# Optimization experiments

Measured on AMD Instinct MI355X. Metric: run time of the kernel, lower is better.

The kernel has to match this reference:

```python
import jax, jax.numpy as jnp
import numpy as np

B, S, H, NH, HD = 8, 1024, 1024, 16, 64
VALID = 512  # valid tokens per sequence (ragged: each seq half-full)
T = B * VALID  # total_nnz
ROPE_THETA = 10000.0
NEG_INF = -1e9


def rotate_half(x):
    x1, x2 = jnp.split(x, 2, axis=-1)
    return jnp.concatenate((-x2, x1), axis=-1)


def setup_inputs() -> dict:
    key = jax.random.key(0)
    k_h, k_qw, k_ow = jax.random.split(key, 3)
    hidden_states = jax.random.normal(k_h, (T, H), jnp.float32)
    # RoPE cos/sin tables at the positions of the unpadded tokens
    inv_freq = 1.0 / (ROPE_THETA ** (np.arange(0, HD, 2, dtype=np.float32) / HD))  # (HD/2,)
    pos = np.tile(np.arange(VALID, dtype=np.float32), B)  # (T,)
    freqs = pos[:, None] * inv_freq[None, :]  # (T, HD/2)
    emb = np.concatenate([freqs, freqs], axis=-1)  # (T, HD)
    cos = jnp.asarray(np.cos(emb))[:, None, :]  # (T, 1, HD) broadcast over heads
    sin = jnp.asarray(np.sin(emb))[:, None, :]
    # indices of valid tokens in the flattened (B*S) padded layout
    indices = jnp.asarray((np.arange(B)[:, None] * S + np.arange(VALID)[None, :]).reshape(-1).astype(np.int64))
    # additive attention bias: 0 for valid keys, -1e9 for padding keys, shape (B,1,1,S)
    key_valid = np.zeros((B, S), dtype=bool)
    key_valid[:, :VALID] = True
    attention_bias = jnp.where(jnp.asarray(key_valid)[:, None, None, :], 0.0, NEG_INF).astype(jnp.float32)
    qkv_w = jax.random.normal(k_qw, (H, 3 * H), jnp.float32) * 0.02
    qkv_b = jnp.zeros((3 * H,), jnp.float32)
    o_w = jax.random.normal(k_ow, (H, H), jnp.float32) * 0.02
    o_b = jnp.zeros((H,), jnp.float32)
    return {"hidden_states": hidden_states, "cos": cos, "sin": sin,
            "attention_bias": attention_bias, "qkv_w": qkv_w, "qkv_b": qkv_b,
            "o_w": o_w, "o_b": o_b, "indices": indices, "batch": B, "seqlen": S}


def reference(hidden_states, cos, sin, attention_bias, qkv_w, qkv_b, o_w, o_b, indices, batch, seqlen):
    # packed QKV projection on unpadded tokens: (T, 3H)
    qkv = hidden_states @ qkv_w + qkv_b
    q, k, v = jnp.split(qkv, 3, axis=-1)
    q = q.reshape(-1, NH, HD)
    k = k.reshape(-1, NH, HD)
    v = v.reshape(-1, NH, HD)
    # rotary position embedding (applied to unpadded q/k)
    q = q * cos + rotate_half(q) * sin
    k = k * cos + rotate_half(k) * sin

    def pad(x):  # (T, NH, HD) -> (B, S, NH, HD), scatter into zero-padded layout
        return jnp.zeros((batch * seqlen, NH, HD), x.dtype).at[indices].set(x).reshape(batch, seqlen, NH, HD)

    qh = pad(q).transpose(0, 2, 1, 3)  # (B, NH, S, HD)
    kh = pad(k).transpose(0, 2, 1, 3)
    vh = pad(v).transpose(0, 2, 1, 3)
    # scaled dot-product attention with additive bias
    scores = jnp.einsum('bhqd,bhkd->bhqk', qh, kh) / jnp.sqrt(jnp.array(HD, qh.dtype)) + attention_bias
    probs = jax.nn.softmax(scores, axis=-1)
    ctx = jnp.einsum('bhqk,bhkd->bhqd', probs, vh)  # (B, NH, S, HD)
    # unpad and merge heads: gather valid rows from flattened (B*S, H)
    out = ctx.transpose(0, 2, 1, 3).reshape(batch * seqlen, NH * HD)[indices]
    return out @ o_w + o_b  # (T, H)
```

## Files before the change

kernel.cpp:

```cpp
#include <hip/hip_runtime.h>

#define T_TOK 4096
#define HDIM  1024
#define NHEAD 16
#define HEADD 64
#define BATCH 8
#define NVALID 512
#define H3    3072

typedef __bf16 bf16;
typedef __attribute__((ext_vector_type(8))) __bf16 bf16x8;
typedef __attribute__((ext_vector_type(4))) __bf16 bf16x4;
typedef __attribute__((ext_vector_type(4))) float f32x4;

__device__ __forceinline__ void load_lds16(const void* g, void* l) {
  __builtin_amdgcn_global_load_lds(
      (const __attribute__((address_space(1))) unsigned int*)g,
      (__attribute__((address_space(3))) unsigned int*)l, 16, 0, 0);
}

__global__ __launch_bounds__(256) void k_cvt(const float* __restrict__ in,
                                             bf16* __restrict__ out) {
  int i = (blockIdx.x * 256 + threadIdx.x) * 4;
  float4 v = *(const float4*)(in + i);
  bf16x4 o;
  o[0] = (bf16)v.x; o[1] = (bf16)v.y; o[2] = (bf16)v.z; o[3] = (bf16)v.w;
  *(bf16x4*)(out + i) = o;
}

__global__ __launch_bounds__(256) void k_tcvt(const float* __restrict__ W,
                                              bf16* __restrict__ Wt,
                                              int K, int N) {
  __shared__ float t[32][33];
  const int ct = blockIdx.x, rt = blockIdx.y;
  const int c = threadIdx.x & 31, r0 = threadIdx.x >> 5;
#pragma unroll
  for (int kk = 0; kk < 4; ++kk) {
    int r = r0 + kk * 8;
    t[r][c] = W[(size_t)(rt * 32 + r) * N + ct * 32 + c];
  }
  __syncthreads();
#pragma unroll
  for (int kk = 0; kk < 4; ++kk) {
    int n = r0 + kk * 8;
    Wt[(size_t)(ct * 32 + n) * K + rt * 32 + c] = (bf16)t[c][n];
  }
}

template <typename OutT>
__global__ __launch_bounds__(256) void k_gemm(const bf16* __restrict__ A,
                                              const bf16* __restrict__ Bt,
                                              const float* __restrict__ bias,
                                              OutT* __restrict__ C,
                                              int M, int N, int K) {
  __shared__ bf16 As[128 * 32];
  __shared__ bf16 Bs[128 * 32];
  const int tid = threadIdx.x;
  const int lane = tid & 63;
  const int wave = tid >> 6;
  const int wr = wave >> 1, wc = wave & 1;
  const int l15 = lane & 15, g = lane >> 4;
  const int row0 = blockIdx.x * 128, col0 = blockIdx.y * 128;

  f32x4 acc[4][4] = {};

  const bf16* Ag = A + (size_t)(row0 + (tid >> 2)) * K + (tid & 3) * 8;
  const bf16* Bg = Bt + (size_t)(col0 + (tid >> 2)) * K + (tid & 3) * 8;
  const int ldsoff = wave * 64 * 8;

  for (int k0 = 0; k0 < K; k0 += 32) {
    __syncthreads();
    load_lds16(Ag + k0, As + ldsoff);
    load_lds16(Ag + k0 + (size_t)64 * K, As + 2048 + ldsoff);
    load_lds16(Bg + k0, Bs + ldsoff);
    load_lds16(Bg + k0 + (size_t)64 * K, Bs + 2048 + ldsoff);
    __syncthreads();

    bf16x8 af[4], bfr[4];
#pragma unroll
    for (int i = 0; i < 4; ++i)
      af[i] = *(const bf16x8*)(As + (wr * 64 + i * 16 + l15) * 32 + g * 8);
#pragma unroll
    for (int j = 0; j < 4; ++j)
      bfr[j] = *(const bf16x8*)(Bs + (wc * 64 + j * 16 + l15) * 32 + g * 8);
#pragma unroll
    for (int i = 0; i < 4; ++i)
#pragma unroll
      for (int j = 0; j < 4; ++j)
        acc[i][j] = __builtin_amdgcn_mfma_f32_16x16x32_bf16(af[i], bfr[j],
                                                            acc[i][j], 0, 0, 0);
  }

#pragma unroll
  for (int i = 0; i < 4; ++i) {
#pragma unroll
    for (int j = 0; j < 4; ++j) {
      int gc = col0 + wc * 64 + j * 16 + l15;
      float bv = bias ? bias[gc] : 0.f;
#pragma unroll
      for (int e = 0; e < 4; ++e) {
        int gr = row0 + wr * 64 + i * 16 + g * 4 + e;
        C[(size_t)gr * N + gc] = (OutT)(acc[i][j][e] + bv);
      }
    }
  }
}

__global__ __launch_bounds__(256) void k_rope(const bf16* __restrict__ qkv,
                                              const float* __restrict__ cosT,
                                              const float* __restrict__ sinT,
                                              bf16* __restrict__ Qr,
                                              bf16* __restrict__ Kr,
                                              bf16* __restrict__ Vt) {
  __shared__ bf16 vt[64][72];
  const int blk = blockIdx.x;
  const int tt = blk & 7, h = (blk >> 3) & 15, b = blk >> 7;
  const int tid = threadIdx.x;
  const int r = tid >> 2, q4 = tid & 3;
  const int d0 = q4 * 8;
  const int t = b * NVALID + tt * 64 + r;
  const size_t qrow = (size_t)t * H3;

  bf16x8 qlo = *(const bf16x8*)(qkv + qrow + h * 64 + d0);
  bf16x8 qhi = *(const bf16x8*)(qkv + qrow + h * 64 + d0 + 32);
  bf16x8 klo = *(const bf16x8*)(qkv + qrow + 1024 + h * 64 + d0);
  bf16x8 khi = *(const bf16x8*)(qkv + qrow + 1024 + h * 64 + d0 + 32);
  bf16x8 vlo = *(const bf16x8*)(qkv + qrow + 2048 + h * 64 + d0);
  bf16x8 vhi = *(const bf16x8*)(qkv + qrow + 2048 + h * 64 + d0 + 32);

  const float* cp = cosT + (size_t)t * 64 + d0;
  const float* sp = sinT + (size_t)t * 64 + d0;
  float clo[8], chi[8], slo[8], shi[8];
  {
    float4 a0 = *(const float4*)cp,        a1 = *(const float4*)(cp + 4);
    float4 b0 = *(const float4*)(cp + 32), b1 = *(const float4*)(cp + 36);
    float4 e0 = *(const float4*)sp,        e1 = *(const float4*)(sp + 4);
    float4 f0 = *(const float4*)(sp + 32), f1 = *(const float4*)(sp + 36);
    clo[0]=a0.x; clo[1]=a0.y; clo[2]=a0.z; clo[3]=a0.w;
    clo[4]=a1.x; clo[5]=a1.y; clo[6]=a1.z; clo[7]=a1.w;
    chi[0]=b0.x; chi[1]=b0.y; chi[2]=b0.z; chi[3]=b0.w;
    chi[4]=b1.x; chi[5]=b1.y; chi[6]=b1.z; chi[7]=b1.w;
    slo[0]=e0.x; slo[1]=e0.y; slo[2]=e0.z; slo[3]=e0.w;
    slo[4]=e1.x; slo[5]=e1.y; slo[6]=e1.z; slo[7]=e1.w;
    shi[0]=f0.x; shi[1]=f0.y; shi[2]=f0.z; shi[3]=f0.w;
    shi[4]=f1.x; shi[5]=f1.y; shi[6]=f1.z; shi[7]=f1.w;
  }

  bf16x8 qo0, qo1, ko0, ko1;
#pragma unroll
  for (int i = 0; i < 8; ++i) {
    float ql = (float)qlo[i], qh = (float)qhi[i];
    float kl = (float)klo[i], kh = (float)khi[i];
    qo0[i] = (bf16)(ql * clo[i] - qh * slo[i]);
    qo1[i] = (bf16)(qh * chi[i] + ql * shi[i]);
    ko0[i] = (bf16)(kl * clo[i] - kh * slo[i]);
    ko1[i] = (bf16)(kh * chi[i] + kl * shi[i]);
  }
  const size_t orow = ((size_t)(b * NHEAD + h) * NVALID + tt * 64 + r) * HEADD;
  *(bf16x8*)(Qr + orow + d0) = qo0;
  *(bf16x8*)(Qr + orow + d0 + 32) = qo1;
  *(bf16x8*)(Kr + orow + d0) = ko0;
  *(bf16x8*)(Kr + orow + d0 + 32) = ko1;

  *(bf16x8*)(&vt[r][d0]) = vlo;
  *(bf16x8*)(&vt[r][d0 + 32]) = vhi;
  __syncthreads();
  const int d = tid >> 2;
  const size_t vbase =
      ((size_t)(b * NHEAD + h) * HEADD + d) * NVALID + tt * 64 + q4 * 16;
  bf16x8 o0, o1;
#pragma unroll
  for (int kk = 0; kk < 8; ++kk) o0[kk] = vt[q4 * 16 + kk][d];
#pragma unroll
  for (int kk = 0; kk < 8; ++kk) o1[kk] = vt[q4 * 16 + 8 + kk][d];
  *(bf16x8*)(Vt + vbase) = o0;
  *(bf16x8*)(Vt + vbase + 8) = o1;
}

__global__ __launch_bounds__(256) void k_attn(const bf16* __restrict__ Qr,
                                              const bf16* __restrict__ Kr,
                                              const bf16* __restrict__ Vt,
                                              bf16* __restrict__ ctx) {
  __shared__ bf16 Ks[128 * 64];
  __shared__ bf16 Vs[64 * 128];
  __shared__ bf16 Ps[4][16 * 136];

  const int blk = blockIdx.x;
  const int qt = blk & 7, h = (blk >> 3) & 15, b = blk >> 7;
  const int tid = threadIdx.x;
  const int lane = tid & 63;
  const int wave = tid >> 6;
  const int l15 = lane & 15, g = lane >> 4;

  const size_t bh = (size_t)(b * NHEAD + h);
  const bf16* Qg = Qr + (bh * NVALID + qt * 64 + wave * 16) * HEADD;
  const bf16* Kg = Kr + bh * NVALID * HEADD;
  const bf16* Vg = Vt + bh * HEADD * NVALID;

  bf16x8 qf0 = *(const bf16x8*)(Qg + l15 * HEADD + g * 8);
  bf16x8 qf1 = *(const bf16x8*)(Qg + l15 * HEADD + 32 + g * 8);

  f32x4 acc[4] = {};
  float mrow[4], srow[4];
#pragma unroll
  for (int e = 0; e < 4; ++e) { mrow[e] = -1e30f; srow[e] = 0.f; }

  const int srK = tid >> 3;
  const int sdK = (tid & 7) << 4;
  const int sdV = tid >> 4;
  const int skV = (tid & 15) << 4;

  bf16* pw = &Ps[wave][0];

  for (int kb = 0; kb < 4; ++kb) {
    __syncthreads();
#pragma unroll
    for (int p = 0; p < 4; ++p) {
      int row = p * 32 + srK;
      int d2 = sdK ^ ((row & 7) << 4);
      load_lds16(Kg + (size_t)(kb * 128 + row) * HEADD + (d2 >> 1),
                 (char*)Ks + (p * 256 + wave * 64) * 16);
    }
#pragma unroll
    for (int p = 0; p < 4; ++p) {
      int d = p * 16 + sdV;
      int k2 = skV ^ ((d & 7) << 4);
      load_lds16(Vg + (size_t)d * NVALID + kb * 128 + (k2 >> 1),
                 (char*)Vs + (p * 256 + wave * 64) * 16);
    }
    __syncthreads();

    f32x4 sc[8];
#pragma unroll
    for (int f = 0; f < 8; ++f) {
      int krow = f * 16 + l15;
      int swz = (krow & 7) << 4;
      const char* kbase = (const char*)Ks + krow * 128;
      bf16x8 kf0 = *(const bf16x8*)(kbase + ((g * 16) ^ swz));
      bf16x8 kf1 = *(const bf16x8*)(kbase + ((g * 16 + 64) ^ swz));
      f32x4 s = {};
      s = __builtin_amdgcn_mfma_f32_16x16x32_bf16(qf0, kf0, s, 0, 0, 0);
      s = __builtin_amdgcn_mfma_f32_16x16x32_bf16(qf1, kf1, s, 0, 0, 0);
      sc[f] = s;
    }

#pragma unroll
    for (int e = 0; e < 4; ++e) {
      float tm = -1e30f;
#pragma unroll
      for (int f = 0; f < 8; ++f) tm = fmaxf(tm, sc[f][e]);
#pragma unroll
      for (int m = 1; m < 16; m <<= 1) tm = fmaxf(tm, __shfl_xor(tm, m, 64));
      tm *= 0.125f;
      float mnew = fmaxf(mrow[e], tm);
      float corr = __expf(mrow[e] - mnew);
      mrow[e] = mnew;
      srow[e] *= corr;
#pragma unroll
      for (int j = 0; j < 4; ++j) acc[j][e] *= corr;
      float rs = 0.f;
#pragma unroll
      for (int f = 0; f < 8; ++f) {
        float p = __expf(sc[f][e] * 0.125f - mnew);
        sc[f][e] = p;
        rs += p;
      }
#pragma unroll
      for (int m = 1; m < 16; m <<= 1) rs += __shfl_xor(rs, m, 64);
      srow[e] += rs;
    }

#pragma unroll
    for (int f = 0; f < 8; ++f)
#pragma unroll
      for (int e = 0; e < 4; ++e)
        pw[(g * 4 + e) * 136 + f * 16 + l15] = (bf16)sc[f][e];

#pragma unroll
    for (int kt = 0; kt < 4; ++kt) {
      bf16x8 pf = *(const bf16x8*)(pw + l15 * 136 + kt * 32 + g * 8);
#pragma unroll
      for (int j = 0; j < 4; ++j) {
        int d = j * 16 + l15;
        int inner = (kt * 64 + g * 16) ^ ((d & 7) << 4);
        bf16x8 vf = *(const bf16x8*)((const char*)Vs + d * 256 + inner);
        acc[j] = __builtin_amdgcn_mfma_f32_16x16x32_bf16(pf, vf, acc[j], 0, 0, 0);
      }
    }
  }

#pragma unroll
  for (int e = 0; e < 4; ++e) {
    float inv = 1.f / srow[e];
    int row = qt * 64 + wave * 16 + g * 4 + e;
    size_t obase = ((size_t)b * NVALID + row) * HDIM + h * HEADD;
#pragma unroll
    for (int j = 0; j < 4; ++j)
      ctx[obase + j * 16 + l15] = (bf16)(acc[j][e] * inv);
  }
}

extern "C" void kernel_launch(void* const* d_in, const int* in_sizes, int n_in,
                              void* d_out, int out_size, void* d_ws, size_t ws_size,
                              hipStream_t stream) {
  const float* hidden = (const float*)d_in[0];
  const float* cosT   = (const float*)d_in[1];
  const float* sinT   = (const float*)d_in[2];
  const float* qkv_w  = (const float*)d_in[4];
  const float* qkv_b  = (const float*)d_in[5];
  const float* o_w    = (const float*)d_in[6];
  const float* o_b    = (const float*)d_in[7];
  float* out = (float*)d_out;

  char* ws = (char*)d_ws;
  const size_t MB = 1024 * 1024;
  bf16* hb  = (bf16*)(ws);
  bf16* w1t = (bf16*)(ws + 8 * MB);
  bf16* w2t = (bf16*)(ws + 14 * MB);
  bf16* qkv = (bf16*)(ws + 16 * MB);
  bf16* Qr  = (bf16*)(ws + 40 * MB);
  bf16* Kr  = (bf16*)(ws + 48 * MB);
  bf16* Vtb = (bf16*)(ws + 56 * MB);
  bf16* ctx = (bf16*)(ws + 16 * MB);

  k_cvt<<<T_TOK * HDIM / 1024, 256, 0, stream>>>(hidden, hb);
  k_tcvt<<<dim3(H3 / 32, HDIM / 32), 256, 0, stream>>>(qkv_w, w1t, HDIM, H3);
  k_tcvt<<<dim3(HDIM / 32, HDIM / 32), 256, 0, stream>>>(o_w, w2t, HDIM, HDIM);
  k_gemm<bf16><<<dim3(T_TOK / 128, H3 / 128), 256, 0, stream>>>(
      hb, w1t, qkv_b, qkv, T_TOK, H3, HDIM);
  k_rope<<<BATCH * NHEAD * 8, 256, 0, stream>>>(qkv, cosT, sinT, Qr, Kr, Vtb);
  k_attn<<<BATCH * NHEAD * 8, 256, 0, stream>>>(Qr, Kr, Vtb, ctx);
  k_gemm<float><<<dim3(T_TOK / 128, HDIM / 128), 256, 0, stream>>>(
      ctx, w2t, o_b, out, T_TOK, HDIM, HDIM);
}
```

Before: 205.7 us.

## Add 256x256 8-wave ping-pong GEMM with swizzled LDS for QKV projection

Adds a new bf16 GEMM kernel with 256x256 tiles, 512 threads, a double-buffered 128 KB LDS of K=64 slices with XOR swizzle, and interleaved staging of the next tiles between four MFMA phases, using setprio and explicit waitcnt/barriers. The QKV projection is switched to this kernel to improve data reuse and overlap global loads with matrix math. The grid for QKV becomes 16x12 = 192 blocks at one block per CU, so some CUs stay idle and the output write is a scattered per-element store.

```diff
diff --git a/kernel.cpp b/kernel.cpp
--- a/kernel.cpp
+++ b/kernel.cpp
@@ -19,6 +19,13 @@
       (__attribute__((address_space(3))) unsigned int*)l, 16, 0, 0);
 }
 
+#define BARRIER() asm volatile("s_barrier" ::: "memory")
+#define LGKM0()                                      \
+  do {                                               \
+    asm volatile("s_waitcnt lgkmcnt(0)" ::: "memory"); \
+    __builtin_amdgcn_sched_barrier(0);               \
+  } while (0)
+
 __global__ __launch_bounds__(256) void k_cvt(const float* __restrict__ in,
                                              bf16* __restrict__ out) {
   int i = (blockIdx.x * 256 + threadIdx.x) * 4;
@@ -44,6 +51,152 @@
   for (int kk = 0; kk < 4; ++kk) {
     int n = r0 + kk * 8;
     Wt[(size_t)(ct * 32 + n) * K + rt * 32 + c] = (bf16)t[c][n];
+  }
+}
+
+template <typename OutT>
+__global__ __launch_bounds__(512, 1) void k_gemm8(const bf16* __restrict__ A,
+                                                  const bf16* __restrict__ Bt,
+                                                  const float* __restrict__ bias,
+                                                  OutT* __restrict__ C,
+                                                  int M, int N, int K) {
+  __shared__ bf16 lds[2][4][128 * 64];
+  const int tid = threadIdx.x;
+  const int lane = tid & 63;
+  const int wid = tid >> 6;
+  const int wm = wid >> 2;
+  const int wn = wid & 3;
+  const int l15 = lane & 15, g = lane >> 4;
+  const int row0 = blockIdx.x * 256, col0 = blockIdx.y * 256;
+
+  const int srow = tid >> 3;
+  const int sbyte = (tid & 7) << 4;
+  const int scol_el = (sbyte ^ ((srow & 7) << 4)) >> 1;
+
+  f32x4 acc[8][4] = {};
+
+  auto stage = [&](int buf, int half, int t) {
+    const bf16* G = (half < 2) ? A : Bt;
+    const int rbase = ((half < 2) ? row0 : col0) + (half & 1) * 128;
+    char* dst = (char*)&lds[buf][half][0];
+#pragma unroll
+    for (int L = 0; L < 2; ++L) {
+      const bf16* src = G + (size_t)(rbase + L * 64 + srow) * K + t * 64 + scol_el;
+      load_lds16(src, dst + L * 8192 + tid * 16);
+    }
+  };
+  auto lda = [&](int buf, int m, int kk) -> bf16x8 {
+    int r = wm * 128 + m * 16 + l15;
+    int rr = r & 127;
+    int byte = rr * 128 + ((kk * 64 + g * 16) ^ ((rr & 7) << 4));
+    return *(const bf16x8*)((const char*)&lds[buf][r >> 7][0] + byte);
+  };
+  auto ldb = [&](int buf, int n, int kk) -> bf16x8 {
+    int r = wn * 64 + n * 16 + l15;
+    int rr = r & 127;
+    int byte = rr * 128 + ((kk * 64 + g * 16) ^ ((rr & 7) << 4));
+    return *(const bf16x8*)((const char*)&lds[buf][2 + (r >> 7)][0] + byte);
+  };
+
+  const int NT = K >> 6;
+
+  stage(0, 0, 0); stage(0, 1, 0); stage(0, 2, 0); stage(0, 3, 0);
+  if (NT > 1) {
+    stage(1, 0, 1); stage(1, 2, 1); stage(1, 3, 1);
+    asm volatile("s_waitcnt vmcnt(6)" ::: "memory");
+  } else {
+    asm volatile("s_waitcnt vmcnt(0)" ::: "memory");
+  }
+  BARRIER();
+
+  bf16x8 af[4][2], bfr[4][2];
+  for (int t = 0; t < NT; ++t) {
+    const int cur = t & 1, nxt = cur ^ 1;
+#pragma unroll
+    for (int n = 0; n < 2; ++n)
+#pragma unroll
+      for (int kk = 0; kk < 2; ++kk) bfr[n][kk] = ldb(cur, n, kk);
+#pragma unroll
+    for (int m = 0; m < 4; ++m)
+#pragma unroll
+      for (int kk = 0; kk < 2; ++kk) af[m][kk] = lda(cur, m, kk);
+    if (t + 1 < NT) stage(nxt, 1, t + 1);
+    BARRIER(); LGKM0();
+    __builtin_amdgcn_s_setprio(1);
+#pragma unroll
+    for (int m = 0; m < 4; ++m)
+#pragma unroll
+      for (int n = 0; n < 2; ++n)
+#pragma unroll
+        for (int kk = 0; kk < 2; ++kk)
+          acc[m][n] = __builtin_amdgcn_mfma_f32_16x16x32_bf16(
+              af[m][kk], bfr[n][kk], acc[m][n], 0, 0, 0);
+    __builtin_amdgcn_s_setprio(0);
+    BARRIER();
+#pragma unroll
+    for (int n = 0; n < 2; ++n)
+#pragma unroll
+      for (int kk = 0; kk < 2; ++kk) bfr[2 + n][kk] = ldb(cur, 2 + n, kk);
+    BARRIER(); LGKM0();
+    __builtin_amdgcn_s_setprio(1);
+#pragma unroll
+    for (int m = 0; m < 4; ++m)
+#pragma unroll
+      for (int n = 0; n < 2; ++n)
+#pragma unroll
+        for (int kk = 0; kk < 2; ++kk)
+          acc[m][2 + n] = __builtin_amdgcn_mfma_f32_16x16x32_bf16(
+              af[m][kk], bfr[2 + n][kk], acc[m][2 + n], 0, 0, 0);
+    __builtin_amdgcn_s_setprio(0);
+    BARRIER();
+#pragma unroll
+    for (int m = 0; m < 4; ++m)
+#pragma unroll
+      for (int kk = 0; kk < 2; ++kk) af[m][kk] = lda(cur, 4 + m, kk);
+    if (t + 2 < NT) { stage(cur, 2, t + 2); stage(cur, 3, t + 2); }
+    BARRIER(); LGKM0();
+    __builtin_amdgcn_s_setprio(1);
+#pragma unroll
+    for (int m = 0; m < 4; ++m)
+#pragma unroll
+      for (int n = 0; n < 2; ++n)
+#pragma unroll
+        for (int kk = 0; kk < 2; ++kk)
+          acc[4 + m][n] = __builtin_amdgcn_mfma_f32_16x16x32_bf16(
+              af[m][kk], bfr[n][kk], acc[4 + m][n], 0, 0, 0);
+    __builtin_amdgcn_s_setprio(0);
+    BARRIER();
+    if (t + 2 < NT) stage(cur, 0, t + 2);
+    __builtin_amdgcn_s_setprio(1);
+#pragma unroll
+    for (int m = 0; m < 4; ++m)
+#pragma unroll
+      for (int n = 0; n < 2; ++n)
+#pragma unroll
+        for (int kk = 0; kk < 2; ++kk)
+          acc[4 + m][2 + n] = __builtin_amdgcn_mfma_f32_16x16x32_bf16(
+              af[m][kk], bfr[2 + n][kk], acc[4 + m][2 + n], 0, 0, 0);
+    __builtin_amdgcn_s_setprio(0);
+    if (t + 2 < NT) {
+      asm volatile("s_waitcnt vmcnt(6)" ::: "memory");
+    } else {
+      asm volatile("s_waitcnt vmcnt(0)" ::: "memory");
+    }
+    BARRIER();
+  }
+
+#pragma unroll
+  for (int m = 0; m < 8; ++m) {
+#pragma unroll
+    for (int n = 0; n < 4; ++n) {
+      int gc = col0 + wn * 64 + n * 16 + l15;
+      float bv = bias ? bias[gc] : 0.f;
+#pragma unroll
+      for (int e = 0; e < 4; ++e) {
+        int gr = row0 + wm * 128 + m * 16 + g * 4 + e;
+        C[(size_t)gr * N + gc] = (OutT)(acc[m][n][e] + bv);
+      }
+    }
   }
 }
 
@@ -326,7 +479,7 @@
   k_cvt<<<T_TOK * HDIM / 1024, 256, 0, stream>>>(hidden, hb);
   k_tcvt<<<dim3(H3 / 32, HDIM / 32), 256, 0, stream>>>(qkv_w, w1t, HDIM, H3);
   k_tcvt<<<dim3(HDIM / 32, HDIM / 32), 256, 0, stream>>>(o_w, w2t, HDIM, HDIM);
-  k_gemm<bf16><<<dim3(T_TOK / 128, H3 / 128), 256, 0, stream>>>(
+  k_gemm8<bf16><<<dim3(T_TOK / 256, H3 / 256), 512, 0, stream>>>(
       hb, w1t, qkv_b, qkv, T_TOK, H3, HDIM);
   k_rope<<<BATCH * NHEAD * 8, 256, 0, stream>>>(qkv, cosT, sinT, Qr, Kr, Vtb);
   k_attn<<<BATCH * NHEAD * 8, 256, 0, stream>>>(Qr, Kr, Vtb, ctx);
```

Measured after the change: 208.0 us. Within noise of the previous version (+1.1%).

## Split-K output projection and pipeline K/V staging in attention

Applied to the files above, without the earlier changes.

The output projection GEMM is split along K into two halves. This doubles the grid from 256 to 512 blocks and fills more CUs, and a separate reduction kernel adds the partial sums and the bias. In the attention kernel, K and V loads into LDS are staged separately: the next K tile is prefetched during the PV MFMAs, and the waits use explicit waitcnt and barriers instead of __syncthreads. The softmax scale is folded into Q, which removes per-score multiplies. In exchange the change costs an extra launch, 32MB of fp32 partial traffic, and a small precision change from rounding the scaled Q to bf16.

```diff
diff --git a/kernel.cpp b/kernel.cpp
--- a/kernel.cpp
+++ b/kernel.cpp
@@ -104,6 +104,77 @@
       }
     }
   }
+}
+
+__global__ __launch_bounds__(256) void k_gemm2k(const bf16* __restrict__ A,
+                                                const bf16* __restrict__ Bt,
+                                                float* __restrict__ Cp,
+                                                int M, int N, int K) {
+  __shared__ bf16 As[128 * 32];
+  __shared__ bf16 Bs[128 * 32];
+  const int tid = threadIdx.x;
+  const int lane = tid & 63;
+  const int wave = tid >> 6;
+  const int wr = wave >> 1, wc = wave & 1;
+  const int l15 = lane & 15, g = lane >> 4;
+  const int row0 = blockIdx.x * 128, col0 = blockIdx.y * 128;
+  const int kbase = blockIdx.z * 512;
+  float* C = Cp + (size_t)blockIdx.z * M * N;
+
+  f32x4 acc[4][4] = {};
+
+  const bf16* Ag = A + (size_t)(row0 + (tid >> 2)) * K + kbase + (tid & 3) * 8;
+  const bf16* Bg = Bt + (size_t)(col0 + (tid >> 2)) * K + kbase + (tid & 3) * 8;
+  const int ldsoff = wave * 64 * 8;
+
+  for (int k0 = 0; k0 < 512; k0 += 32) {
+    __syncthreads();
+    load_lds16(Ag + k0, As + ldsoff);
+    load_lds16(Ag + k0 + (size_t)64 * K, As + 2048 + ldsoff);
+    load_lds16(Bg + k0, Bs + ldsoff);
+    load_lds16(Bg + k0 + (size_t)64 * K, Bs + 2048 + ldsoff);
+    __syncthreads();
+
+    bf16x8 af[4], bfr[4];
+#pragma unroll
+    for (int i = 0; i < 4; ++i)
+      af[i] = *(const bf16x8*)(As + (wr * 64 + i * 16 + l15) * 32 + g * 8);
+#pragma unroll
+    for (int j = 0; j < 4; ++j)
+      bfr[j] = *(const bf16x8*)(Bs + (wc * 64 + j * 16 + l15) * 32 + g * 8);
+#pragma unroll
+    for (int i = 0; i < 4; ++i)
+#pragma unroll
+      for (int j = 0; j < 4; ++j)
+        acc[i][j] = __builtin_amdgcn_mfma_f32_16x16x32_bf16(af[i], bfr[j],
+                                                            acc[i][j], 0, 0, 0);
+  }
+
+#pragma unroll
+  for (int i = 0; i < 4; ++i)
+#pragma unroll
+    for (int j = 0; j < 4; ++j) {
+      int gc = col0 + wc * 64 + j * 16 + l15;
+#pragma unroll
+      for (int e = 0; e < 4; ++e) {
+        int gr = row0 + wr * 64 + i * 16 + g * 4 + e;
+        C[(size_t)gr * N + gc] = acc[i][j][e];
+      }
+    }
+}
+
+__global__ __launch_bounds__(256) void k_red(const float* __restrict__ p0,
+                                             const float* __restrict__ p1,
+                                             const float* __restrict__ bias,
+                                             float* __restrict__ out) {
+  int i4 = blockIdx.x * 256 + threadIdx.x;
+  float4 a = *(const float4*)(p0 + (size_t)i4 * 4);
+  float4 b = *(const float4*)(p1 + (size_t)i4 * 4);
+  float4 bv = *(const float4*)(bias + ((i4 * 4) & (HDIM - 1)));
+  float4 o;
+  o.x = a.x + b.x + bv.x; o.y = a.y + b.y + bv.y;
+  o.z = a.z + b.z + bv.z; o.w = a.w + b.w + bv.w;
+  *(float4*)(out + (size_t)i4 * 4) = o;
 }
 
 __global__ __launch_bounds__(256) void k_rope(const bf16* __restrict__ qkv,
@@ -199,6 +270,11 @@
 
   bf16x8 qf0 = *(const bf16x8*)(Qg + l15 * HEADD + g * 8);
   bf16x8 qf1 = *(const bf16x8*)(Qg + l15 * HEADD + 32 + g * 8);
+#pragma unroll
+  for (int i = 0; i < 8; ++i) {
+    qf0[i] = (bf16)((float)qf0[i] * 0.125f);
+    qf1[i] = (bf16)((float)qf1[i] * 0.125f);
+  }
 
   f32x4 acc[4] = {};
   float mrow[4], srow[4];
@@ -212,8 +288,7 @@
 
   bf16* pw = &Ps[wave][0];
 
-  for (int kb = 0; kb < 4; ++kb) {
-    __syncthreads();
+  auto stageK = [&](int kb) {
 #pragma unroll
     for (int p = 0; p < 4; ++p) {
       int row = p * 32 + srK;
@@ -221,6 +296,8 @@
       load_lds16(Kg + (size_t)(kb * 128 + row) * HEADD + (d2 >> 1),
                  (char*)Ks + (p * 256 + wave * 64) * 16);
     }
+  };
+  auto stageV = [&](int kb) {
 #pragma unroll
     for (int p = 0; p < 4; ++p) {
       int d = p * 16 + sdV;
@@ -228,7 +305,16 @@
       load_lds16(Vg + (size_t)d * NVALID + kb * 128 + (k2 >> 1),
                  (char*)Vs + (p * 256 + wave * 64) * 16);
     }
-    __syncthreads();
+  };
+
+  stageK(0);
+
+  for (int kb = 0; kb < 4; ++kb) {
+    asm volatile("s_waitcnt lgkmcnt(0)" ::: "memory");
+    __builtin_amdgcn_s_barrier();
+    stageV(kb);
+    asm volatile("s_waitcnt vmcnt(4)" ::: "memory");
+    __builtin_amdgcn_s_barrier();
 
     f32x4 sc[8];
 #pragma unroll
@@ -251,7 +337,6 @@
       for (int f = 0; f < 8; ++f) tm = fmaxf(tm, sc[f][e]);
 #pragma unroll
       for (int m = 1; m < 16; m <<= 1) tm = fmaxf(tm, __shfl_xor(tm, m, 64));
-      tm *= 0.125f;
       float mnew = fmaxf(mrow[e], tm);
       float corr = __expf(mrow[e] - mnew);
       mrow[e] = mnew;
@@ -261,7 +346,7 @@
       float rs = 0.f;
 #pragma unroll
       for (int f = 0; f < 8; ++f) {
-        float p = __expf(sc[f][e] * 0.125f - mnew);
+        float p = __expf(sc[f][e] - mnew);
         sc[f][e] = p;
         rs += p;
       }
@@ -275,6 +360,11 @@
 #pragma unroll
       for (int e = 0; e < 4; ++e)
         pw[(g * 4 + e) * 136 + f * 16 + l15] = (bf16)sc[f][e];
+
+    asm volatile("s_waitcnt vmcnt(0)" ::: "memory");
+    __builtin_amdgcn_s_barrier();
+
+    if (kb < 3) stageK(kb + 1);
 
 #pragma unroll
     for (int kt = 0; kt < 4; ++kt) {
@@ -314,14 +404,15 @@
 
   char* ws = (char*)d_ws;
   const size_t MB = 1024 * 1024;
-  bf16* hb  = (bf16*)(ws);
-  bf16* w1t = (bf16*)(ws + 8 * MB);
-  bf16* w2t = (bf16*)(ws + 14 * MB);
-  bf16* qkv = (bf16*)(ws + 16 * MB);
-  bf16* Qr  = (bf16*)(ws + 40 * MB);
-  bf16* Kr  = (bf16*)(ws + 48 * MB);
-  bf16* Vtb = (bf16*)(ws + 56 * MB);
-  bf16* ctx = (bf16*)(ws + 16 * MB);
+  bf16*  hb  = (bf16*)(ws);
+  bf16*  w1t = (bf16*)(ws + 8 * MB);
+  bf16*  w2t = (bf16*)(ws + 14 * MB);
+  bf16*  qkv = (bf16*)(ws + 16 * MB);
+  bf16*  Qr  = (bf16*)(ws + 40 * MB);
+  bf16*  Kr  = (bf16*)(ws + 48 * MB);
+  bf16*  Vtb = (bf16*)(ws + 56 * MB);
+  bf16*  ctx = (bf16*)(ws + 16 * MB);
+  float* cp0 = (float*)(ws + 80 * MB);
 
   k_cvt<<<T_TOK * HDIM / 1024, 256, 0, stream>>>(hidden, hb);
   k_tcvt<<<dim3(H3 / 32, HDIM / 32), 256, 0, stream>>>(qkv_w, w1t, HDIM, H3);
@@ -330,6 +421,8 @@
       hb, w1t, qkv_b, qkv, T_TOK, H3, HDIM);
   k_rope<<<BATCH * NHEAD * 8, 256, 0, stream>>>(qkv, cosT, sinT, Qr, Kr, Vtb);
   k_attn<<<BATCH * NHEAD * 8, 256, 0, stream>>>(Qr, Kr, Vtb, ctx);
-  k_gemm<float><<<dim3(T_TOK / 128, HDIM / 128), 256, 0, stream>>>(
-      ctx, w2t, o_b, out, T_TOK, HDIM, HDIM);
-}
+  k_gemm2k<<<dim3(T_TOK / 128, HDIM / 128, 2), 256, 0, stream>>>(
+      ctx, w2t, cp0, T_TOK, HDIM, HDIM);
+  k_red<<<T_TOK * HDIM / 1024, 256, 0, stream>>>(
+      cp0, cp0 + (size_t)T_TOK * HDIM, o_b, out);
+}
```

After: 203.6 us. No clear change (-1.0%).
